# Performance work log

Hardware: AMD Instinct MI355X
Metric: run time of the kernel (lower is better)

The kernel has to match this reference:

```python
import jax, jax.numpy as jnp
import numpy as np


def setup_inputs() -> dict:
    key = jax.random.key(0)
    k1, k2, k3, k4, k5 = jax.random.split(key, 5)
    B, S, D, U = 64, 2048, 512, 512
    he = lambda k, shape: jax.random.normal(k, shape, dtype=jnp.float32) * jnp.sqrt(2.0 / shape[0])
    return {
        "query": jax.random.normal(k1, (B, D), dtype=jnp.float32),
        "values": jax.random.normal(k2, (B, S, D), dtype=jnp.float32),
        "W1": he(k3, (D, U)),
        "W2": he(k4, (D, U)),
        "V1": he(k5, (U, 1)),
    }


def reference(query, values, W1, W2, V1):
    # query: (B, D), values: (B, S, D)
    Q = query @ W1                       # (B, U)
    V = jnp.einsum("bsd,du->bsu", values, W2)  # (B, S, U)
    add = jnp.tanh(Q[:, None, :] + V)    # (B, S, U)
    score = jnp.einsum("bsu,uo->bso", add, V1)  # (B, S, 1)
    attn = jax.nn.softmax(score, axis=1)         # (B, S, 1)
    context = jnp.sum(attn * values, axis=1)     # (B, D)
    return context
```

## Files before the change

kernel.cpp:

```cpp
#include <hip/hip_runtime.h>


typedef __attribute__((ext_vector_type(8))) short bf16x8;
typedef __attribute__((ext_vector_type(4))) float f32x4;

#if __has_builtin(__builtin_amdgcn_exp2f)
__device__ __forceinline__ float fast_exp2(float x) { return __builtin_amdgcn_exp2f(x); }
#else
__device__ __forceinline__ float fast_exp2(float x) { return exp2f(x); }
#endif
#if __has_builtin(__builtin_amdgcn_rcpf)
__device__ __forceinline__ float fast_rcp(float x) { return __builtin_amdgcn_rcpf(x); }
#else
__device__ __forceinline__ float fast_rcp(float x) { return 1.0f / x; }
#endif

__device__ __forceinline__ unsigned short f2bf(float f) {
  unsigned int u = __float_as_uint(f);
  u += 0x7fffu + ((u >> 16) & 1u);
  return (unsigned short)(u >> 16);
}

__device__ __forceinline__ void async16(const void* g, void* l) {
  __builtin_amdgcn_global_load_lds(
      (const __attribute__((address_space(1))) unsigned int*)g,
      (__attribute__((address_space(3))) unsigned int*)l, 16, 0, 0);
}

__global__ void qk(const float* __restrict__ query, const float* __restrict__ W1,
                   float* __restrict__ Q) {
  __shared__ float qrow[512];
  const int b = blockIdx.x, t = threadIdx.x;
  qrow[t] = query[b * 512 + t];
  qrow[t + 256] = query[b * 512 + t + 256];
  __syncthreads();
  float a0 = 0.f, a1 = 0.f;
  for (int k = 0; k < 512; ++k) {
    const float q = qrow[k];
    const float* w = W1 + (size_t)k * 512;
    a0 += q * w[t];
    a1 += q * w[t + 256];
  }
  Q[b * 512 + t] = a0;
  Q[b * 512 + t + 256] = a1;
}

__global__ void wt_k(const float* __restrict__ W2, unsigned short* __restrict__ Wt) {
  __shared__ float tile[32][33];
  const int k0 = blockIdx.x * 32, n0 = blockIdx.y * 32;
  const int tx = threadIdx.x, ty = threadIdx.y;
  for (int i = 0; i < 32; i += 8)
    tile[ty + i][tx] = W2[(size_t)(k0 + ty + i) * 512 + n0 + tx];
  __syncthreads();
  for (int i = 0; i < 32; i += 8)
    Wt[(size_t)(n0 + ty + i) * 512 + k0 + tx] = f2bf(tile[tx][ty + i]);
}

__global__ __launch_bounds__(512, 2) void scores_k(
    const float* __restrict__ values, const unsigned short* __restrict__ Wt,
    const float* __restrict__ Q, const float* __restrict__ V1,
    float* __restrict__ scores) {
  __shared__ __align__(16) unsigned short Ab[64 * 512];
  __shared__ __align__(16) unsigned short Bb[512 * 64];
  __shared__ float sAcc[64];

  const int t = threadIdx.x;
  const int lane = t & 63;
  const int w = t >> 6;
  const int quad = lane >> 4;
  const int l15 = lane & 15;
  const int m0 = blockIdx.x * 64;
  const int b = m0 >> 11;

  if (t < 64) sAcc[t] = 0.0f;

  const float* Ag = values + (size_t)m0 * 512;
#pragma unroll
  for (int i = 0; i < 8; ++i) {
    const int c = i * 512 + t;
    const int m = c >> 6;
    const int kc = c & 63;
    const float4* src = (const float4*)(Ag + (size_t)m * 512 + kc * 8);
    const float4 x = src[0], y = src[1];
    const unsigned int p0 = (unsigned int)f2bf(x.x) | ((unsigned int)f2bf(x.y) << 16);
    const unsigned int p1 = (unsigned int)f2bf(x.z) | ((unsigned int)f2bf(x.w) << 16);
    const unsigned int p2 = (unsigned int)f2bf(y.x) | ((unsigned int)f2bf(y.y) << 16);
    const unsigned int p3 = (unsigned int)f2bf(y.z) | ((unsigned int)f2bf(y.w) << 16);
    *(uint4*)&Ab[m * 512 + ((kc ^ (m & 7)) * 8)] = make_uint4(p0, p1, p2, p3);
  }

  f32x4 acc[4][4];
#pragma unroll
  for (int mt = 0; mt < 4; ++mt)
#pragma unroll
    for (int nt = 0; nt < 4; ++nt) acc[mt][nt] = (f32x4){0.f, 0.f, 0.f, 0.f};

  for (int piece = 0; piece < 8; ++piece) {
    __syncthreads();
#pragma unroll
    for (int j = 0; j < 8; ++j) {
      const int nb = w * 64 + j * 8;
      const int n = nb + (lane >> 3);
      const int kcc = (lane & 7) ^ (n & 7);
      const unsigned short* g = Wt + (size_t)n * 512 + piece * 64 + kcc * 8;
      async16(g, &Bb[nb * 64]);
    }
    __syncthreads();

#pragma unroll
    for (int ksl = 0; ksl < 2; ++ksl) {
      bf16x8 af[4], bfr[4];
      const int kc = piece * 8 + ksl * 4 + quad;
      const int kcc = ksl * 4 + quad;
#pragma unroll
      for (int mt = 0; mt < 4; ++mt) {
        const int m = mt * 16 + l15;
        af[mt] = *(const bf16x8*)&Ab[m * 512 + ((kc ^ (m & 7)) * 8)];
      }
#pragma unroll
      for (int nt = 0; nt < 4; ++nt) {
        const int n = w * 64 + nt * 16 + l15;
        bfr[nt] = *(const bf16x8*)&Bb[n * 64 + ((kcc ^ (n & 7)) * 8)];
      }
#pragma unroll
      for (int mt = 0; mt < 4; ++mt)
#pragma unroll
        for (int nt = 0; nt < 4; ++nt)
          acc[mt][nt] = __builtin_amdgcn_mfma_f32_16x16x32_bf16(af[mt], bfr[nt],
                                                                acc[mt][nt], 0, 0, 0);
    }
  }

  float part[4][4];
#pragma unroll
  for (int mt = 0; mt < 4; ++mt)
#pragma unroll
    for (int r = 0; r < 4; ++r) part[mt][r] = 0.f;

#pragma unroll
  for (int nt = 0; nt < 4; ++nt) {
    const int n = w * 64 + nt * 16 + l15;
    const float qv = Q[b * 512 + n];
    const float v1 = V1[n];
#pragma unroll
    for (int mt = 0; mt < 4; ++mt)
#pragma unroll
      for (int r = 0; r < 4; ++r) {
        const float x = acc[mt][nt][r] + qv;
        const float e = fast_exp2(x * 2.8853900817779268f);
        const float th = 1.0f - 2.0f * fast_rcp(e + 1.0f);
        part[mt][r] += th * v1;
      }
  }
#pragma unroll
  for (int mt = 0; mt < 4; ++mt)
#pragma unroll
    for (int r = 0; r < 4; ++r) {
      float v = part[mt][r];
      v += __shfl_xor(v, 1);
      v += __shfl_xor(v, 2);
      v += __shfl_xor(v, 4);
      v += __shfl_xor(v, 8);
      if (l15 == 0) atomicAdd(&sAcc[mt * 16 + quad * 4 + r], v);
    }
  __syncthreads();
  if (t < 64) scores[m0 + t] = sAcc[t];
}

__global__ void softmax_k(float* __restrict__ scores) {
  __shared__ float red[8];
  const int bq = blockIdx.x, t = threadIdx.x;
  float* s = scores + (size_t)bq * 2048;
  float v[8];
  float mx = -3.0e38f;
#pragma unroll
  for (int i = 0; i < 8; ++i) {
    v[i] = s[t + i * 256];
    mx = fmaxf(mx, v[i]);
  }
#pragma unroll
  for (int o = 1; o < 64; o <<= 1) mx = fmaxf(mx, __shfl_xor(mx, o));
  if ((t & 63) == 0) red[t >> 6] = mx;
  __syncthreads();
  mx = fmaxf(fmaxf(red[0], red[1]), fmaxf(red[2], red[3]));
  float e[8];
  float sum = 0.f;
#pragma unroll
  for (int i = 0; i < 8; ++i) {
    e[i] = fast_exp2((v[i] - mx) * 1.4426950408889634f);
    sum += e[i];
  }
#pragma unroll
  for (int o = 1; o < 64; o <<= 1) sum += __shfl_xor(sum, o);
  if ((t & 63) == 0) red[4 + (t >> 6)] = sum;
  __syncthreads();
  const float inv = 1.0f / (red[4] + red[5] + red[6] + red[7]);
#pragma unroll
  for (int i = 0; i < 8; ++i) s[t + i * 256] = e[i] * inv;
}

__global__ __launch_bounds__(1024) void ctx_k(const float* __restrict__ values,
                                              const float* __restrict__ attn,
                                              float* __restrict__ out) {
  __shared__ float red[1024];
  const int bid = blockIdx.x;
  const int b = bid >> 2, dc = bid & 3;
  const int t = threadIdx.x;
  const int d = dc * 128 + (t & 127);
  const int sg = t >> 7;
  const float* vb = values + (size_t)b * 2048 * 512;
  const float* ab = attn + (size_t)b * 2048;
  float acc = 0.f;
#pragma unroll 4
  for (int s = sg; s < 2048; s += 8) acc += ab[s] * vb[(size_t)s * 512 + d];
  red[t] = acc;
  __syncthreads();
  if (t < 128) {
    float r = 0.f;
#pragma unroll
    for (int i = 0; i < 8; ++i) r += red[t + i * 128];
    out[b * 512 + dc * 128 + t] = r;
  }
}

extern "C" void kernel_launch(void* const* d_in, const int* in_sizes, int n_in,
                              void* d_out, int out_size, void* d_ws, size_t ws_size,
                              hipStream_t stream) {
  const float* query = (const float*)d_in[0];
  const float* values = (const float*)d_in[1];
  const float* W1 = (const float*)d_in[2];
  const float* W2 = (const float*)d_in[3];
  const float* V1 = (const float*)d_in[4];
  float* out = (float*)d_out;

  char* ws = (char*)d_ws;
  float* Qp = (float*)ws;
  unsigned short* Wtp = (unsigned short*)(ws + 131072);
  float* Sp = (float*)(ws + 131072 + 524288);

  qk<<<64, 256, 0, stream>>>(query, W1, Qp);
  wt_k<<<dim3(16, 16), dim3(32, 8), 0, stream>>>(W2, Wtp);
  scores_k<<<2048, 512, 0, stream>>>(values, Wtp, Qp, V1, Sp);
  softmax_k<<<64, 256, 0, stream>>>(Sp);
  ctx_k<<<256, 1024, 0, stream>>>(values, Sp, out);
}
```

Measured before the change: 557.2 us.

## Load W2 fragments directly from global, raise occupancy, split ctx over sequence chunks

The scores kernel stops staging W2 tiles through shared memory with async copies and per-piece barriers. Each wave now reads its B fragments straight from global/L2, which frees 64KB of LDS so the launch bound can request four blocks per CU. The context kernel is split into eight sequence chunks per batch that combine with float atomics into an output zeroed by the softmax kernel. The Q projection is also spread over twice as many blocks. The risks are uncoalesced 16-byte global reads of W2 in the inner loop and nondeterministic atomic summation order.

Result: faster. 528.6 us (-5.1%).

```diff
diff --git a/kernel.cpp b/kernel.cpp
--- a/kernel.cpp
+++ b/kernel.cpp
@@ -21,28 +21,18 @@
   return (unsigned short)(u >> 16);
 }
 
-__device__ __forceinline__ void async16(const void* g, void* l) {
-  __builtin_amdgcn_global_load_lds(
-      (const __attribute__((address_space(1))) unsigned int*)g,
-      (__attribute__((address_space(3))) unsigned int*)l, 16, 0, 0);
-}
-
 __global__ void qk(const float* __restrict__ query, const float* __restrict__ W1,
                    float* __restrict__ Q) {
   __shared__ float qrow[512];
-  const int b = blockIdx.x, t = threadIdx.x;
+  const int b = blockIdx.x, half = blockIdx.y, t = threadIdx.x;
   qrow[t] = query[b * 512 + t];
   qrow[t + 256] = query[b * 512 + t + 256];
   __syncthreads();
-  float a0 = 0.f, a1 = 0.f;
-  for (int k = 0; k < 512; ++k) {
-    const float q = qrow[k];
-    const float* w = W1 + (size_t)k * 512;
-    a0 += q * w[t];
-    a1 += q * w[t + 256];
-  }
-  Q[b * 512 + t] = a0;
-  Q[b * 512 + t + 256] = a1;
+  const int u = half * 256 + t;
+  float acc = 0.f;
+#pragma unroll 8
+  for (int k = 0; k < 512; ++k) acc += qrow[k] * W1[(size_t)k * 512 + u];
+  Q[b * 512 + u] = acc;
 }
 
 __global__ void wt_k(const float* __restrict__ W2, unsigned short* __restrict__ Wt) {
@@ -56,12 +46,11 @@
     Wt[(size_t)(n0 + ty + i) * 512 + k0 + tx] = f2bf(tile[tx][ty + i]);
 }
 
-__global__ __launch_bounds__(512, 2) void scores_k(
+__global__ __launch_bounds__(512, 4) void scores_k(
     const float* __restrict__ values, const unsigned short* __restrict__ Wt,
     const float* __restrict__ Q, const float* __restrict__ V1,
     float* __restrict__ scores) {
   __shared__ __align__(16) unsigned short Ab[64 * 512];
-  __shared__ __align__(16) unsigned short Bb[512 * 64];
   __shared__ float sAcc[64];
 
   const int t = threadIdx.x;
@@ -88,6 +77,7 @@
     const unsigned int p3 = (unsigned int)f2bf(y.z) | ((unsigned int)f2bf(y.w) << 16);
     *(uint4*)&Ab[m * 512 + ((kc ^ (m & 7)) * 8)] = make_uint4(p0, p1, p2, p3);
   }
+  __syncthreads();
 
   f32x4 acc[4][4];
 #pragma unroll
@@ -95,40 +85,26 @@
 #pragma unroll
     for (int nt = 0; nt < 4; ++nt) acc[mt][nt] = (f32x4){0.f, 0.f, 0.f, 0.f};
 
-  for (int piece = 0; piece < 8; ++piece) {
-    __syncthreads();
-#pragma unroll
-    for (int j = 0; j < 8; ++j) {
-      const int nb = w * 64 + j * 8;
-      const int n = nb + (lane >> 3);
-      const int kcc = (lane & 7) ^ (n & 7);
-      const unsigned short* g = Wt + (size_t)n * 512 + piece * 64 + kcc * 8;
-      async16(g, &Bb[nb * 64]);
+  const unsigned short* Bg = Wt + (size_t)(w * 64 + l15) * 512 + quad * 8;
+  const int sw = l15 & 7;
+
+#pragma unroll
+  for (int ks = 0; ks < 16; ++ks) {
+    bf16x8 bfr[4], af[4];
+#pragma unroll
+    for (int nt = 0; nt < 4; ++nt)
+      bfr[nt] = *(const bf16x8*)(Bg + nt * (16 * 512) + ks * 32);
+#pragma unroll
+    for (int mt = 0; mt < 4; ++mt) {
+      const int m = mt * 16 + l15;
+      af[mt] = *(const bf16x8*)&Ab[m * 512 + (((ks * 4 + quad) ^ sw) * 8)];
     }
-    __syncthreads();
-
-#pragma unroll
-    for (int ksl = 0; ksl < 2; ++ksl) {
-      bf16x8 af[4], bfr[4];
-      const int kc = piece * 8 + ksl * 4 + quad;
-      const int kcc = ksl * 4 + quad;
-#pragma unroll
-      for (int mt = 0; mt < 4; ++mt) {
-        const int m = mt * 16 + l15;
-        af[mt] = *(const bf16x8*)&Ab[m * 512 + ((kc ^ (m & 7)) * 8)];
-      }
-#pragma unroll
-      for (int nt = 0; nt < 4; ++nt) {
-        const int n = w * 64 + nt * 16 + l15;
-        bfr[nt] = *(const bf16x8*)&Bb[n * 64 + ((kcc ^ (n & 7)) * 8)];
-      }
-#pragma unroll
-      for (int mt = 0; mt < 4; ++mt)
-#pragma unroll
-        for (int nt = 0; nt < 4; ++nt)
-          acc[mt][nt] = __builtin_amdgcn_mfma_f32_16x16x32_bf16(af[mt], bfr[nt],
-                                                                acc[mt][nt], 0, 0, 0);
-    }
+#pragma unroll
+    for (int mt = 0; mt < 4; ++mt)
+#pragma unroll
+      for (int nt = 0; nt < 4; ++nt)
+        acc[mt][nt] = __builtin_amdgcn_mfma_f32_16x16x32_bf16(af[mt], bfr[nt],
+                                                              acc[mt][nt], 0, 0, 0);
   }
 
   float part[4][4];
@@ -167,9 +143,11 @@
   if (t < 64) scores[m0 + t] = sAcc[t];
 }
 
-__global__ void softmax_k(float* __restrict__ scores) {
+__global__ void softmax_k(float* __restrict__ scores, float* __restrict__ out) {
   __shared__ float red[8];
   const int bq = blockIdx.x, t = threadIdx.x;
+  out[bq * 512 + t] = 0.f;
+  out[bq * 512 + 256 + t] = 0.f;
   float* s = scores + (size_t)bq * 2048;
   float v[8];
   float mx = -3.0e38f;
@@ -199,28 +177,18 @@
   for (int i = 0; i < 8; ++i) s[t + i * 256] = e[i] * inv;
 }
 
-__global__ __launch_bounds__(1024) void ctx_k(const float* __restrict__ values,
-                                              const float* __restrict__ attn,
-                                              float* __restrict__ out) {
-  __shared__ float red[1024];
+__global__ __launch_bounds__(512) void ctx_k(const float* __restrict__ values,
+                                             const float* __restrict__ attn,
+                                             float* __restrict__ out) {
   const int bid = blockIdx.x;
-  const int b = bid >> 2, dc = bid & 3;
+  const int b = bid >> 3, sc = bid & 7;
   const int t = threadIdx.x;
-  const int d = dc * 128 + (t & 127);
-  const int sg = t >> 7;
-  const float* vb = values + (size_t)b * 2048 * 512;
-  const float* ab = attn + (size_t)b * 2048;
+  const float* vb = values + (size_t)b * 2048 * 512 + (size_t)sc * 256 * 512;
+  const float* ab = attn + (size_t)b * 2048 + sc * 256;
   float acc = 0.f;
-#pragma unroll 4
-  for (int s = sg; s < 2048; s += 8) acc += ab[s] * vb[(size_t)s * 512 + d];
-  red[t] = acc;
-  __syncthreads();
-  if (t < 128) {
-    float r = 0.f;
-#pragma unroll
-    for (int i = 0; i < 8; ++i) r += red[t + i * 128];
-    out[b * 512 + dc * 128 + t] = r;
-  }
+#pragma unroll 8
+  for (int s = 0; s < 256; ++s) acc += ab[s] * vb[(size_t)s * 512 + t];
+  atomicAdd(&out[b * 512 + t], acc);
 }
 
 extern "C" void kernel_launch(void* const* d_in, const int* in_sizes, int n_in,
@@ -238,9 +206,9 @@
   unsigned short* Wtp = (unsigned short*)(ws + 131072);
   float* Sp = (float*)(ws + 131072 + 524288);
 
-  qk<<<64, 256, 0, stream>>>(query, W1, Qp);
+  qk<<<dim3(64, 2), 256, 0, stream>>>(query, W1, Qp);
   wt_k<<<dim3(16, 16), dim3(32, 8), 0, stream>>>(W2, Wtp);
   scores_k<<<2048, 512, 0, stream>>>(values, Wtp, Qp, V1, Sp);
-  softmax_k<<<64, 256, 0, stream>>>(Sp);
-  ctx_k<<<256, 1024, 0, stream>>>(values, Sp, out);
-}
+  softmax_k<<<64, 256, 0, stream>>>(Sp, out);
+  ctx_k<<<512, 512, 0, stream>>>(values, Sp, out);
+}
```
